# Kernel tuning notes

Measured on AMD Instinct MI355X. Metric: run time of the kernel, lower is better.

## Reference

```python
import jax, jax.numpy as jnp
import numpy as np

N_NODES = 100000
N_EDGES = 3200000
F_IN = 512
F_HID = 32
N_CLASSES = 16


def gcn_conv(x, edge_index, W, b):
    """PyG GCNConv: symmetric-normalized aggregation with self-loops.
    out_i = sum_{j->i} (d_j d_i)^{-1/2} (x_j W) + d_i^{-1} (x_i W) + b
    where d_i = in-degree(i) + 1 (self-loop included)."""
    n = x.shape[0]
    h = x @ W  # [N, F_out]
    src, dst = edge_index[0], edge_index[1]
    deg = jax.ops.segment_sum(jnp.ones_like(src, dtype=h.dtype), dst,
                              num_segments=n) + 1.0  # self-loop
    dinv = jax.lax.rsqrt(deg)  # [N]
    norm = dinv[src] * dinv[dst]  # [E]
    msg = h[src] * norm[:, None]  # [E, F_out]
    agg = jax.ops.segment_sum(msg, dst, num_segments=n)
    # self-loop contribution: norm_ii = dinv_i^2
    agg = agg + h * (dinv * dinv)[:, None]
    return agg + b


def setup_inputs() -> dict:
    key = jax.random.key(0)
    k1, k2, k3, k4 = jax.random.split(key, 4)
    x = jax.random.normal(k1, (N_NODES, F_IN), dtype=jnp.float32)
    edge_index = jax.random.randint(k2, (2, N_EDGES), 0, N_NODES, dtype=jnp.int64)
    W1 = jax.random.normal(k3, (F_IN, F_HID), dtype=jnp.float32) / np.sqrt(F_IN)
    b1 = jnp.zeros((F_HID,), dtype=jnp.float32)
    W2 = jax.random.normal(k4, (F_HID, N_CLASSES), dtype=jnp.float32) / np.sqrt(F_HID)
    b2 = jnp.zeros((N_CLASSES,), dtype=jnp.float32)
    return {"x": x, "edge_index": edge_index, "W1": W1, "b1": b1, "W2": W2, "b2": b2}


def reference(x, edge_index, W1, b1, W2, b2):
    h = jax.nn.relu(gcn_conv(x, edge_index, W1, b1))
    # F.dropout(training=self.training) is identity in eval mode
    h = gcn_conv(h, edge_index, W2, b2)
    return jax.nn.log_softmax(h, axis=1)
```

## Files before the change

### kernel.cpp

```cpp
#include <hip/hip_runtime.h>
#include <cstdint>
#include <cstddef>

#define F_IN 512
#define F_HID 32
#define N_CLS 16
#define BSH 9
#define BNODES (1 << BSH)
#define CAP 20480
#define SK 16

typedef __attribute__((ext_vector_type(4))) float f32x4;
typedef __attribute__((ext_vector_type(8))) __bf16 bf16x8;

__device__ __forceinline__ float4 shfl_xor_f4(float4 v, int mask) {
    v.x = __shfl_xor(v.x, mask, 64);
    v.y = __shfl_xor(v.y, mask, 64);
    v.z = __shfl_xor(v.z, mask, 64);
    v.w = __shfl_xor(v.w, mask, 64);
    return v;
}

__device__ __forceinline__ short bf16s(float f) {
    unsigned u = __float_as_uint(f);
    return (short)((u + 0x7FFFu + ((u >> 16) & 1u)) >> 16);
}
__device__ __forceinline__ unsigned pack2(float a, float b) {
    return (unsigned)(unsigned short)bf16s(a) | ((unsigned)(unsigned short)bf16s(b) << 16);
}
__device__ __forceinline__ float bf_lo(unsigned p) { return __uint_as_float(p << 16); }
__device__ __forceinline__ float bf_hi(unsigned p) { return __uint_as_float(p & 0xFFFF0000u); }

__global__ __launch_bounds__(256) void k_detect(const int* e, int* flag, int* bcur,
                                                int nbuk) {
    __shared__ int zc;
    int t = threadIdx.x;
    if (t == 0) zc = 0;
    __syncthreads();
    int z = 0;
#pragma unroll
    for (int j = 0; j < 4; ++j)
        if (e[2 * (t * 4 + j) + 1] == 0) z++;
    if (z) atomicAdd(&zc, z);
    for (int i = t; i < nbuk; i += 256) bcur[i] = i * CAP;
    __syncthreads();
    if (t == 0) *flag = (zc >= 1016) ? 1 : 0;
}

__global__ __launch_bounds__(256) void k_wcvt(const float* __restrict__ W,
                                              uint4* __restrict__ Wfrag) {
    int i = blockIdx.x * 256 + threadIdx.x;
    int s = i >> 7, rem = i & 127, h = rem >> 6, l = rem & 63;
    int g = l >> 4, c = 16 * h + (l & 15);
    unsigned p[4];
#pragma unroll
    for (int q = 0; q < 4; ++q) {
        int base = (q < 2) ? (4 * g + 2 * q) : (16 + 4 * g + 2 * (q - 2));
        int k0 = 32 * s + base;
        unsigned lo = (unsigned short)bf16s(W[(size_t)k0 * F_HID + c]);
        unsigned hi = (unsigned short)bf16s(W[(size_t)(k0 + 1) * F_HID + c]);
        p[q] = lo | (hi << 16);
    }
    Wfrag[i] = make_uint4(p[0], p[1], p[2], p[3]);
}

__device__ __forceinline__ int edge_get(const void* e, int is64, long long idx) {
    return is64 ? (int)((const long long*)e)[idx] : ((const int*)e)[idx];
}

__global__ __launch_bounds__(256) void k_fused(const float* __restrict__ x,
                                               const uint4* __restrict__ Wfrag,
                                               float* __restrict__ hs1, int N,
                                               const void* edges, const int* flag,
                                               int* bcur, int* __restrict__ bucket,
                                               int E, int nbuk, int SB) {
    __shared__ uint4 wf[2048];
    int t = threadIdx.x;

    if ((int)blockIdx.x < SB) {
        int* h = (int*)wf;
        int* sbase = h + 256;
        if (t < nbuk) h[t] = 0;
        __syncthreads();
        int is64 = *flag;
        long long base = (long long)blockIdx.x * 256 * SK;
        int ss[SK], dd[SK], rk[SK];
#pragma unroll
        for (int j = 0; j < SK; ++j) {
            long long i = base + j * 256 + t;
            if (i < E) {
                dd[j] = edge_get(edges, is64, (long long)E + i);
                ss[j] = edge_get(edges, is64, i);
                rk[j] = atomicAdd(&h[dd[j] >> BSH], 1);
            } else dd[j] = -1;
        }
        __syncthreads();
        if (t < nbuk && h[t]) sbase[t] = atomicAdd(&bcur[t], h[t]);
        __syncthreads();
#pragma unroll
        for (int j = 0; j < SK; ++j) {
            if (dd[j] >= 0) {
                int b = dd[j] >> BSH;
                int pos = sbase[b] + rk[j];
                if (pos < (b + 1) * CAP)
                    bucket[pos] = ((dd[j] & (BNODES - 1)) << 17) | ss[j];
            }
        }
    } else {
#pragma unroll
        for (int j = 0; j < 8; ++j) wf[t + j * 256] = Wfrag[t + j * 256];
        __syncthreads();
        int tile = blockIdx.x - SB;
        int w = t >> 6, l = t & 63;
        int c = l & 15, g = l >> 4;
        int wrow = tile * 64 + w * 16;
        int row = wrow + c;
        if (row >= N) row = N - 1;
        const float4* xpA = (const float4*)(x + (size_t)row * F_IN + 4 * g);
        const float4* xpB = (const float4*)(x + (size_t)row * F_IN + 16 + 4 * g);

        f32x4 acc0 = {0.f, 0.f, 0.f, 0.f};
        f32x4 acc1 = {0.f, 0.f, 0.f, 0.f};

        float4 A[4], B[4];
#pragma unroll
        for (int j = 0; j < 4; ++j) { A[j] = xpA[8 * j]; B[j] = xpB[8 * j]; }

#pragma unroll
        for (int s = 0; s < 16; ++s) {
            const int j = s & 3;
            float4 a0 = A[j], a1 = B[j];
            if (s < 12) { A[j] = xpA[8 * (s + 4)]; B[j] = xpB[8 * (s + 4)]; }
            bf16x8 av;
            av[0] = (__bf16)a0.x; av[1] = (__bf16)a0.y;
            av[2] = (__bf16)a0.z; av[3] = (__bf16)a0.w;
            av[4] = (__bf16)a1.x; av[5] = (__bf16)a1.y;
            av[6] = (__bf16)a1.z; av[7] = (__bf16)a1.w;
            bf16x8 b0 = __builtin_bit_cast(bf16x8, wf[s * 128 + l]);
            bf16x8 b1 = __builtin_bit_cast(bf16x8, wf[s * 128 + 64 + l]);
            acc0 = __builtin_amdgcn_mfma_f32_16x16x32_bf16(av, b0, acc0, 0, 0, 0);
            acc1 = __builtin_amdgcn_mfma_f32_16x16x32_bf16(av, b1, acc1, 0, 0, 0);
        }

#pragma unroll
        for (int r = 0; r < 4; ++r) {
            int ro = wrow + g * 4 + r;
            if (ro < N) {
                hs1[(size_t)ro * F_HID + c]      = acc0[r];
                hs1[(size_t)ro * F_HID + 16 + c] = acc1[r];
            }
        }
    }
}

__global__ __launch_bounds__(512) void k_build(const int* __restrict__ bucket,
                                               const int* __restrict__ bcur,
                                               int* __restrict__ rbeg,
                                               int* __restrict__ rend,
                                               float* __restrict__ dinv,
                                               int* __restrict__ csr,
                                               const float* __restrict__ hs1,
                                               uint2* __restrict__ hs1b, int N) {
    __shared__ int cnt[512];
    __shared__ int wsum[8];
    __shared__ float sdinv[512];
    int b = blockIdx.x;
    int t = threadIdx.x;
    int nb0 = b << BSH;
    int beg = b * CAP, end = bcur[b];
    cnt[t] = 0;
    __syncthreads();
    for (int e = beg + t; e < end; e += 512)
        atomicAdd(&cnt[bucket[e] >> 17], 1);
    __syncthreads();
    int v = cnt[t];
    int lane = t & 63, w = t >> 6;
    int inc = v;
#pragma unroll
    for (int off = 1; off < 64; off <<= 1) {
        int u = __shfl_up(inc, off, 64);
        if (lane >= off) inc += u;
    }
    if (lane == 63) wsum[w] = inc;
    __syncthreads();
    int wo = 0;
#pragma unroll
    for (int k = 0; k < 8; ++k)
        if (k < w) wo += wsum[k];
    int excl = inc - v + wo;
    int node = nb0 + t;
    float d = rsqrtf((float)v + 1.0f);
    sdinv[t] = d;
    if (node < N) {
        rbeg[node] = beg + excl;
        rend[node] = beg + excl + v;
        dinv[node] = d;
    }
    __syncthreads();
    cnt[t] = beg + excl;
    __syncthreads();
    for (int e = beg + t; e < end; e += 512) {
        int p = bucket[e];
        int pos = atomicAdd(&cnt[p >> 17], 1);
        csr[pos] = p & 0x1FFFF;
    }
    const float4* h1 = (const float4*)hs1 + (size_t)nb0 * 8;
    uint2* hb = hs1b + (size_t)nb0 * 8;
    for (int j = t; j < 4096; j += 512) {
        int n2 = nb0 + (j >> 3);
        if (n2 < N) {
            float dv = sdinv[j >> 3];
            float4 vv = h1[j];
            hb[j] = make_uint2(pack2(vv.x * dv, vv.y * dv),
                               pack2(vv.z * dv, vv.w * dv));
        }
    }
}

__global__ __launch_bounds__(256) void k_gather1(const uint2* __restrict__ hs1b,
                                                 const int* __restrict__ csr,
                                                 const int* __restrict__ rbeg,
                                                 const int* __restrict__ rend,
                                                 const float* __restrict__ dinv,
                                                 const float* __restrict__ b1,
                                                 const float* __restrict__ W2,
                                                 float* __restrict__ hs2, int N) {
    __shared__ float w2s[32][17];
    int t = threadIdx.x;
    for (int i = t; i < 512; i += 256) w2s[i >> 4][i & 15] = W2[i];
    __syncthreads();
    int node = blockIdx.x * 4 + (t >> 6);
    if (node >= N) return;
    int lane = t & 63;
    int g = lane >> 3, l = lane & 7;
    int beg = rbeg[node], end = rend[node];
    float4 a = make_float4(0.f, 0.f, 0.f, 0.f);
    int e = beg + g;
    int nsrc = (e < end) ? csr[e] : 0;
    for (; e < end; e += 8) {
        int src = nsrc;
        if (e + 8 < end) nsrc = csr[e + 8];
        uint2 q = hs1b[(size_t)src * 8 + l];
        a.x += bf_lo(q.x); a.y += bf_hi(q.x);
        a.z += bf_lo(q.y); a.w += bf_hi(q.y);
    }
    float4 u;
    u = shfl_xor_f4(a, 8);  a.x += u.x; a.y += u.y; a.z += u.z; a.w += u.w;
    u = shfl_xor_f4(a, 16); a.x += u.x; a.y += u.y; a.z += u.z; a.w += u.w;
    u = shfl_xor_f4(a, 32); a.x += u.x; a.y += u.y; a.z += u.z; a.w += u.w;
    uint2 sq = hs1b[(size_t)node * 8 + l];
    float di = dinv[node];
    float4 bb = ((const float4*)b1)[l];
    float4 r;
    r.x = fmaxf(di * (a.x + bf_lo(sq.x)) + bb.x, 0.f);
    r.y = fmaxf(di * (a.y + bf_hi(sq.x)) + bb.y, 0.f);
    r.z = fmaxf(di * (a.z + bf_lo(sq.y)) + bb.z, 0.f);
    r.w = fmaxf(di * (a.w + bf_hi(sq.y)) + bb.w, 0.f);
    int k0 = 4 * l, c0 = 2 * g;
    float p0 = r.x * w2s[k0][c0]     + r.y * w2s[k0 + 1][c0]
             + r.z * w2s[k0 + 2][c0] + r.w * w2s[k0 + 3][c0];
    float p1 = r.x * w2s[k0][c0 + 1]     + r.y * w2s[k0 + 1][c0 + 1]
             + r.z * w2s[k0 + 2][c0 + 1] + r.w * w2s[k0 + 3][c0 + 1];
    p0 += __shfl_xor(p0, 1, 64); p1 += __shfl_xor(p1, 1, 64);
    p0 += __shfl_xor(p0, 2, 64); p1 += __shfl_xor(p1, 2, 64);
    p0 += __shfl_xor(p0, 4, 64); p1 += __shfl_xor(p1, 4, 64);
    if (l == 0)
        *(float2*)(hs2 + (size_t)node * N_CLS + c0) = make_float2(p0 * di, p1 * di);
}

__global__ __launch_bounds__(256) void k_gather2(const float* __restrict__ hs2,
                                                 const int* __restrict__ csr,
                                                 const int* __restrict__ rbeg,
                                                 const int* __restrict__ rend,
                                                 const float* __restrict__ dinv,
                                                 const float* __restrict__ b2,
                                                 float* __restrict__ out, int N) {
    int node = blockIdx.x * 4 + (threadIdx.x >> 6);
    if (node >= N) return;
    int lane = threadIdx.x & 63;
    int g = lane >> 2, l = lane & 3;
    const float4* h4 = (const float4*)hs2;
    int beg = rbeg[node], end = rend[node];
    float4 a = make_float4(0.f, 0.f, 0.f, 0.f);
    int e = beg + g;
    int nsrc = (e < end) ? csr[e] : 0;
    for (; e < end; e += 16) {
        int src = nsrc;
        if (e + 16 < end) nsrc = csr[e + 16];
        float4 v = h4[(size_t)src * 4 + l];
        a.x += v.x; a.y += v.y; a.z += v.z; a.w += v.w;
    }
    float4 u;
    u = shfl_xor_f4(a, 4);  a.x += u.x; a.y += u.y; a.z += u.z; a.w += u.w;
    u = shfl_xor_f4(a, 8);  a.x += u.x; a.y += u.y; a.z += u.z; a.w += u.w;
    u = shfl_xor_f4(a, 16); a.x += u.x; a.y += u.y; a.z += u.z; a.w += u.w;
    u = shfl_xor_f4(a, 32); a.x += u.x; a.y += u.y; a.z += u.z; a.w += u.w;
    if (g == 0) {
        float4 self = h4[(size_t)node * 4 + l];
        float di = dinv[node];
        float4 bb = ((const float4*)b2)[l];
        float4 v;
        v.x = di * (a.x + self.x) + bb.x;
        v.y = di * (a.y + self.y) + bb.y;
        v.z = di * (a.z + self.z) + bb.z;
        v.w = di * (a.w + self.w) + bb.w;
        float m = fmaxf(fmaxf(v.x, v.y), fmaxf(v.z, v.w));
        m = fmaxf(m, __shfl_xor(m, 1, 64));
        m = fmaxf(m, __shfl_xor(m, 2, 64));
        float s = __expf(v.x - m) + __expf(v.y - m) + __expf(v.z - m) + __expf(v.w - m);
        s += __shfl_xor(s, 1, 64);
        s += __shfl_xor(s, 2, 64);
        float ls = m + __logf(s);
        float4 r = make_float4(v.x - ls, v.y - ls, v.z - ls, v.w - ls);
        ((float4*)out)[(size_t)node * 4 + l] = r;
    }
}

extern "C" void kernel_launch(void* const* d_in, const int* in_sizes, int n_in,
                              void* d_out, int out_size, void* d_ws, size_t ws_size,
                              hipStream_t stream) {
    const float* x  = (const float*)d_in[0];
    const void* edges = d_in[1];
    const float* W1 = (const float*)d_in[2];
    const float* b1 = (const float*)d_in[3];
    const float* W2 = (const float*)d_in[4];
    const float* b2 = (const float*)d_in[5];
    float* out = (float*)d_out;

    const int N = in_sizes[0] / F_IN;
    const int E = in_sizes[1] / 2;
    const int NBUK = (N + BNODES - 1) >> BSH;

    char* w = (char*)d_ws;
    size_t off = 0;
    auto take = [&](size_t bytes) {
        size_t o = off;
        off += (bytes + 15) & ~(size_t)15;
        return o;
    };
    float* hs1    = (float*)(w + take((size_t)N * F_HID * 4));
    uint2* hs1b   = (uint2*)(w + take((size_t)N * 8 * 8));
    float* hs2    = (float*)(w + take((size_t)N * N_CLS * 4));
    float* dinv   = (float*)(w + take((size_t)N * 4));
    int* rbeg     = (int*)(w + take((size_t)N * 4));
    int* rend     = (int*)(w + take((size_t)N * 4));
    int* bucket   = (int*)(w + take((size_t)NBUK * CAP * 4));
    int* csr      = (int*)(w + take((size_t)NBUK * CAP * 4));
    uint4* Wfrag  = (uint4*)(w + take(2048 * 16));
    int* bcur     = (int*)(w + take(1024));
    int* flag     = (int*)(w + take(16));

    hipLaunchKernelGGL(k_detect, dim3(1), dim3(256), 0, stream, (const int*)edges, flag, bcur, NBUK);
    hipLaunchKernelGGL(k_wcvt, dim3(8), dim3(256), 0, stream, W1, Wfrag);
    const int SB = (E + 256 * SK - 1) / (256 * SK);
    const int NT = (N + 63) / 64;
    hipLaunchKernelGGL(k_fused, dim3(SB + NT), dim3(256), 0, stream,
                       x, Wfrag, hs1, N, edges, flag, bcur, bucket, E, NBUK, SB);
    hipLaunchKernelGGL(k_build, dim3(NBUK), dim3(512), 0, stream, bucket, bcur, rbeg, rend, dinv, csr, hs1, hs1b, N);
    hipLaunchKernelGGL(k_gather1, dim3((N + 3) / 4), dim3(256), 0, stream, hs1b, csr, rbeg, rend, dinv, b1, W2, hs2, N);
    hipLaunchKernelGGL(k_gather2, dim3((N + 3) / 4), dim3(256), 0, stream, hs2, csr, rbeg, rend, dinv, b2, out, N);
}
```

Measured before the change: 201.0 us.

## Stage x tiles into LDS via async global_load_lds with double buffering

The GEMM part of the fused kernel now streams x rows into a per-wave LDS double buffer using direct global-to-LDS loads with an XOR swizzle, instead of holding a register prefetch queue of float4 loads. Each step waits on vmcnt, reads A fragments from LDS, runs the MFMAs and then issues the loads two steps ahead. The intent is more coalesced x reads and lower register pressure. In exchange it adds 16KB of LDS per block, which may reduce occupancy, and the manual waitcnt ordering is fragile.

```diff
diff --git a/kernel.cpp b/kernel.cpp
--- a/kernel.cpp
+++ b/kernel.cpp
@@ -13,6 +13,10 @@
 typedef __attribute__((ext_vector_type(4))) float f32x4;
 typedef __attribute__((ext_vector_type(8))) __bf16 bf16x8;
 
+#define GLDS16(gp, lp) __builtin_amdgcn_global_load_lds( \
+    (const __attribute__((address_space(1))) void*)(gp), \
+    (__attribute__((address_space(3))) void*)(lp), 16, 0, 0)
+
 __device__ __forceinline__ float4 shfl_xor_f4(float4 v, int mask) {
     v.x = __shfl_xor(v.x, mask, 64);
     v.y = __shfl_xor(v.y, mask, 64);
@@ -75,6 +79,7 @@
                                                int* bcur, int* __restrict__ bucket,
                                                int E, int nbuk, int SB) {
     __shared__ uint4 wf[2048];
+    __shared__ float4 xs[4][2][128];
     int t = threadIdx.x;
 
     if ((int)blockIdx.x < SB) {
@@ -111,26 +116,39 @@
         for (int j = 0; j < 8; ++j) wf[t + j * 256] = Wfrag[t + j * 256];
         __syncthreads();
         int tile = blockIdx.x - SB;
-        int w = t >> 6, l = t & 63;
+        int wv = t >> 6, l = t & 63;
         int c = l & 15, g = l >> 4;
-        int wrow = tile * 64 + w * 16;
-        int row = wrow + c;
-        if (row >= N) row = N - 1;
-        const float4* xpA = (const float4*)(x + (size_t)row * F_IN + 4 * g);
-        const float4* xpB = (const float4*)(x + (size_t)row * F_IN + 16 + 4 * g);
+        int wrow = tile * 64 + wv * 16;
+        char* xw = (char*)&xs[wv][0][0];
+
+        auto STAGE = [&](int buf, int s) {
+#pragma unroll
+            for (int j = 0; j < 2; ++j) {
+                int i = l + j * 64;
+                int rr = i >> 3, kk = i & 7;
+                int grow = wrow + rr;
+                if (grow >= N) grow = N - 1;
+                const float* gp = x + (size_t)grow * F_IN + s * 32 + ((kk ^ (rr & 7)) << 2);
+                GLDS16(gp, xw + buf * 2048 + j * 1024);
+            }
+        };
 
         f32x4 acc0 = {0.f, 0.f, 0.f, 0.f};
         f32x4 acc1 = {0.f, 0.f, 0.f, 0.f};
-
-        float4 A[4], B[4];
-#pragma unroll
-        for (int j = 0; j < 4; ++j) { A[j] = xpA[8 * j]; B[j] = xpB[8 * j]; }
+        STAGE(0, 0);
+        STAGE(1, 1);
+        const int p1 = g ^ (c & 7);
+        const int p2 = (g + 4) ^ (c & 7);
+        const float4* xb0 = (const float4*)xw + c * 8;
+        const float4* xb1 = (const float4*)(xw + 2048) + c * 8;
 
 #pragma unroll
         for (int s = 0; s < 16; ++s) {
-            const int j = s & 3;
-            float4 a0 = A[j], a1 = B[j];
-            if (s < 12) { A[j] = xpA[8 * (s + 4)]; B[j] = xpB[8 * (s + 4)]; }
+            if (s < 15) asm volatile("s_waitcnt vmcnt(2)" ::: "memory");
+            else        asm volatile("s_waitcnt vmcnt(0)" ::: "memory");
+            const float4* xb = (s & 1) ? xb1 : xb0;
+            float4 a0 = xb[p1];
+            float4 a1 = xb[p2];
             bf16x8 av;
             av[0] = (__bf16)a0.x; av[1] = (__bf16)a0.y;
             av[2] = (__bf16)a0.z; av[3] = (__bf16)a0.w;
@@ -140,6 +158,7 @@
             bf16x8 b1 = __builtin_bit_cast(bf16x8, wf[s * 128 + 64 + l]);
             acc0 = __builtin_amdgcn_mfma_f32_16x16x32_bf16(av, b0, acc0, 0, 0, 0);
             acc1 = __builtin_amdgcn_mfma_f32_16x16x32_bf16(av, b1, acc1, 0, 0, 0);
+            if (s < 14) STAGE(s & 1, s + 2);
         }
 
 #pragma unroll
@@ -357,6 +376,8 @@
     hipLaunchKernelGGL(k_fused, dim3(SB + NT), dim3(256), 0, stream,
                        x, Wfrag, hs1, N, edges, flag, bcur, bucket, E, NBUK, SB);
     hipLaunchKernelGGL(k_build, dim3(NBUK), dim3(512), 0, stream, bucket, bcur, rbeg, rend, dinv, csr, hs1, hs1b, N);
-    hipLaunchKernelGGL(k_gather1, dim3((N + 3) / 4), dim3(256), 0, stream, hs1b, csr, rbeg, rend, dinv, b1, W2, hs2, N);
-    hipLaunchKernelGGL(k_gather2, dim3((N + 3) / 4), dim3(256), 0, stream, hs2, csr, rbeg, rend, dinv, b2, out, N);
-}
+    hipLaunchKernelGGL(k_gather1, dim3((N + 3) / 4), dim3(256), 0, stream,
+                       hs1b, csr, rbeg, rend, dinv, b1, W2, hs2, N);
+    hipLaunchKernelGGL(k_gather2, dim3((N + 3) / 4), dim3(256), 0, stream,
+                       hs2, csr, rbeg, rend, dinv, b2, out, N);
+}
```

After: 217.5 us. 1.08x slower.
